# Optimization experiments

Hardware: AMD Instinct MI355X
Metric: run time of the kernel (lower is better)

The kernel has to match this reference:

```python
import jax, jax.numpy as jnp
import numpy as np

N_NODES = 100000
N_EDGES = 3200000
K_HOPS = 10
ALPHA = 0.1


def setup_inputs() -> dict:
    key = jax.random.key(0)
    ks = jax.random.split(key, 7)
    x = jax.random.normal(ks[0], (N_NODES, 500), dtype=jnp.float32)
    edge_index = jax.random.randint(ks[1], (2, N_EDGES), 0, N_NODES, dtype=jnp.int32)
    W1 = jax.random.normal(ks[2], (500, 64), dtype=jnp.float32) * 0.05
    b1 = jax.random.normal(ks[3], (64,), dtype=jnp.float32) * 0.05
    W2 = jax.random.normal(ks[4], (64, 64), dtype=jnp.float32) * 0.1
    b2 = jax.random.normal(ks[5], (64,), dtype=jnp.float32) * 0.05
    # PPR init: temp[k] = alpha*(1-alpha)^k, temp[K] = (1-alpha)^K
    temp = ALPHA * (1.0 - ALPHA) ** np.arange(K_HOPS + 1)
    temp[-1] = (1.0 - ALPHA) ** K_HOPS
    temp = jnp.asarray(temp, dtype=jnp.float32)
    return {"x": x, "edge_index": edge_index, "W1": W1, "b1": b1,
            "W2": W2, "b2": b2, "temp": temp}


def reference(x, edge_index, W1, b1, W2, b2, temp):
    n = x.shape[0]
    # MLP (dropout is identity in eval mode)
    h = jax.nn.relu(x @ W1 + b1)
    h = h @ W2 + b2  # [N, C]

    # gcn_norm with self-loops (edge_weight=None -> all ones)
    loops = jnp.arange(n, dtype=edge_index.dtype)
    row = jnp.concatenate([edge_index[0], loops])  # source (x_j)
    col = jnp.concatenate([edge_index[1], loops])  # target (aggregate)
    w = jnp.ones(row.shape[0], dtype=h.dtype)
    deg = jax.ops.segment_sum(w, col, num_segments=n)
    dinv = jnp.where(deg > 0, jax.lax.rsqrt(deg), 0.0)
    norm = dinv[row] * w * dinv[col]  # [E+N]

    # GPR propagation: hidden = sum_k temp[k] * A_hat^k h
    hidden = h * temp[0]
    cur = h
    for k in range(K_HOPS):
        cur = jax.ops.segment_sum(norm[:, None] * cur[row], col, num_segments=n)
        hidden = hidden + temp[k + 1] * cur

    return jax.nn.log_softmax(hidden, axis=1)
```

## Files before the change

### kernel.cpp

```cpp
#include <hip/hip_runtime.h>
#include <hip/hip_bf16.h>
#include <math.h>

#define FEAT_IN 500
#define HID 64
#define NPB 128
#define MAXB 1024

typedef unsigned int uint;
typedef unsigned short ushort;
typedef __attribute__((ext_vector_type(8))) short bf16x8;
typedef __attribute__((ext_vector_type(4))) float f32x4;

__device__ inline ushort f2bf(float f) {
    uint u = __float_as_uint(f);
    uint r = (u + 0x7fff + ((u >> 16) & 1)) >> 16;
    return (ushort)r;
}

__device__ inline uint pk2(float a, float b) {
    uint ua = __float_as_uint(a), ub = __float_as_uint(b);
    ua = ua + 0x7fff + ((ua >> 16) & 1);
    ub = ub + 0x7fff + ((ub >> 16) & 1);
    return (ua >> 16) | (ub & 0xffff0000u);
}

__device__ inline void bf8_unpack(const uint4 v, float f[8]) {
    f[0] = __uint_as_float(v.x << 16);
    f[1] = __uint_as_float(v.x & 0xffff0000u);
    f[2] = __uint_as_float(v.y << 16);
    f[3] = __uint_as_float(v.y & 0xffff0000u);
    f[4] = __uint_as_float(v.z << 16);
    f[5] = __uint_as_float(v.z & 0xffff0000u);
    f[6] = __uint_as_float(v.w << 16);
    f[7] = __uint_as_float(v.w & 0xffff0000u);
}

__global__ __launch_bounds__(256) void bcnt_kernel(const int* __restrict__ col,
                                                   int* __restrict__ bcnt, int E, int nbkt) {
    __shared__ int cnt[MAXB];
    int tid = threadIdx.x;
    for (int j = tid; j < nbkt; j += 256) cnt[j] = 0;
    __syncthreads();
    int stride = gridDim.x * 256;
    for (int e = blockIdx.x * 256 + tid; e < E; e += stride) {
        atomicAdd(&cnt[col[e] >> 7], 1);
    }
    __syncthreads();
    for (int j = tid; j < nbkt; j += 256) {
        int v = cnt[j];
        if (v) atomicAdd(&bcnt[j], v);
    }
}

__global__ void bscan_kernel(const int* __restrict__ bcnt, int* __restrict__ boff,
                             int* __restrict__ bcur, int* __restrict__ ptr,
                             int nbkt, int n, int E) {
    int lane = threadIdx.x;
    int run = 0;
    for (int base = 0; base < nbkt; base += 64) {
        int i = base + lane;
        int v = (i < nbkt) ? bcnt[i] : 0;
        int sc = v;
#pragma unroll
        for (int d = 1; d < 64; d <<= 1) {
            int t = __shfl_up(sc, d);
            if (lane >= d) sc += t;
        }
        if (i < nbkt) {
            int ex = run + sc - v;
            boff[i] = ex;
            bcur[i] = ex;
        }
        run += __shfl(sc, 63);
    }
    if (lane == 0) {
        boff[nbkt] = E;
        ptr[n] = E;
    }
}

__global__ __launch_bounds__(1024) void bscat_kernel(const int* __restrict__ row,
                                                     const int* __restrict__ col,
                                                     int* __restrict__ bcur,
                                                     uint* __restrict__ csr_tmp,
                                                     int E, int nbkt) {
    __shared__ int cnt[MAXB];
    __shared__ int pos[MAXB];
    int tid = threadIdx.x;
    int chunk = (E + gridDim.x - 1) / gridDim.x;
    int c0 = blockIdx.x * chunk;
    int c1 = min(E, c0 + chunk);
    for (int j = tid; j < nbkt; j += 1024) cnt[j] = 0;
    __syncthreads();
    for (int e = c0 + tid; e < c1; e += 1024) atomicAdd(&cnt[col[e] >> 7], 1);
    __syncthreads();
    for (int j = tid; j < nbkt; j += 1024) {
        int v = cnt[j];
        pos[j] = v ? atomicAdd(&bcur[j], v) : 0;
    }
    __syncthreads();
    for (int e = c0 + tid; e < c1; e += 1024) {
        int c = col[e];
        int j = c >> 7;
        int r = atomicAdd(&pos[j], 1);
        csr_tmp[r] = ((uint)row[e] << 7) | (uint)(c & (NPB - 1));
    }
}

__global__ __launch_bounds__(256) void bsort_kernel(const uint* __restrict__ csr_tmp,
                                                    const int* __restrict__ boff,
                                                    int* __restrict__ ptr,
                                                    float* __restrict__ dinv,
                                                    int* __restrict__ csr_src,
                                                    int n) {
    __shared__ int degl[NPB];
    __shared__ int offl[NPB];
    int b = blockIdx.x;
    int tid = threadIdx.x;
    int t0 = boff[b], t1 = boff[b + 1];
    if (tid < NPB) degl[tid] = 0;
    __syncthreads();
    for (int p = t0 + tid; p < t1; p += 256) {
        uint pk = csr_tmp[p];
        atomicAdd(&degl[pk & (NPB - 1)], 1);
    }
    __syncthreads();
    if (tid < 64) {
        int v0 = degl[tid];
        int s0 = v0;
#pragma unroll
        for (int d = 1; d < 64; d <<= 1) {
            int t = __shfl_up(s0, d);
            if (tid >= d) s0 += t;
        }
        int tot0 = __shfl(s0, 63);
        int v1 = degl[64 + tid];
        int s1 = v1;
#pragma unroll
        for (int d = 1; d < 64; d <<= 1) {
            int t = __shfl_up(s1, d);
            if (tid >= d) s1 += t;
        }
        offl[tid] = s0 - v0;
        offl[64 + tid] = tot0 + s1 - v1;
    }
    __syncthreads();
    if (tid < NPB) {
        int node = b * NPB + tid;
        if (node < n) {
            ptr[node] = t0 + offl[tid];
            dinv[node] = rsqrtf((float)(degl[tid] + 1));
        }
    }
    __syncthreads();
    for (int p = t0 + tid; p < t1; p += 256) {
        uint pk = csr_tmp[p];
        int l = pk & (NPB - 1);
        int r = t0 + atomicAdd(&offl[l], 1);
        csr_src[r] = (int)(pk >> 7);
    }
}

__global__ void swz_kernel(const float* __restrict__ W1, const float* __restrict__ W2,
                           ushort* __restrict__ w1s, ushort* __restrict__ w2s) {
    int idx = blockIdx.x * blockDim.x + threadIdx.x;
    if (idx < 32768) {
        int j = idx & 7;
        int l = (idx >> 3) & 63;
        int t = (idx >> 9) & 3;
        int c = idx >> 11;
        int k = c * 32 + (l >> 4) * 8 + j;
        int nn = t * 16 + (l & 15);
        float v = (k < FEAT_IN) ? W1[(size_t)k * HID + nn] : 0.0f;
        w1s[idx] = f2bf(v);
    } else if (idx < 32768 + 4096) {
        int r = idx - 32768;
        int j = r & 7;
        int l = (r >> 3) & 63;
        int t = (r >> 9) & 3;
        int c = r >> 11;
        int k = c * 32 + (l >> 4) * 8 + j;
        int nn = t * 16 + (l & 15);
        w2s[r] = f2bf(W2[(size_t)k * HID + nn]);
    }
}

__global__ __launch_bounds__(256) void mlp_kernel(const float* __restrict__ x,
                                                  const ushort* __restrict__ w1s,
                                                  const float* __restrict__ b1,
                                                  const ushort* __restrict__ w2s,
                                                  const float* __restrict__ b2,
                                                  const float* __restrict__ temp,
                                                  const float* __restrict__ dinv,
                                                  ushort* __restrict__ A,
                                                  float* __restrict__ out, int n) {
    __shared__ float pacc[2][2][16][65];
    __shared__ ushort hls[2][16 * 72];
    const int tid = threadIdx.x;
    const int lane = tid & 63;
    const int wv = tid >> 6;
    const int tl = wv >> 1;
    const int kh = wv & 1;
    const int g = lane >> 4;
    const int c15 = lane & 15;
    const int nmt = (n + 15) / 16;
    int mt = blockIdx.x * 2 + tl;
    bool mtok = (mt < nmt);
    float t0 = temp[0];

    f32x4 acc[4] = {{0.f, 0.f, 0.f, 0.f}, {0.f, 0.f, 0.f, 0.f},
                    {0.f, 0.f, 0.f, 0.f}, {0.f, 0.f, 0.f, 0.f}};
    int row = mt * 16 + c15;
    bool rok = mtok && (row < n);
    const float* xr = x + (size_t)row * FEAT_IN;

    if (mtok) {
        const int cbeg = kh * 8;
        const int cend = kh ? 15 : 8;
        float4 L0 = {0.f, 0.f, 0.f, 0.f}, H0 = L0, L1 = L0, H1 = L0;
        if (rok) {
            L0 = *(const float4*)(xr + cbeg * 32 + g * 8);
            H0 = *(const float4*)(xr + cbeg * 32 + g * 8 + 4);
            L1 = *(const float4*)(xr + (cbeg + 1) * 32 + g * 8);
            H1 = *(const float4*)(xr + (cbeg + 1) * 32 + g * 8 + 4);
        }
        for (int c = cbeg; c < cend; c++) {
            float4 Ln = {0.f, 0.f, 0.f, 0.f}, Hn = Ln;
            int cn = c + 2;
            if (rok && cn < cend) {
                Ln = *(const float4*)(xr + cn * 32 + g * 8);
                Hn = *(const float4*)(xr + cn * 32 + g * 8 + 4);
            }
            uint4 au;
            au.x = pk2(L0.x, L0.y);
            au.y = pk2(L0.z, L0.w);
            au.z = pk2(H0.x, H0.y);
            au.w = pk2(H0.z, H0.w);
            bf16x8 a = *(bf16x8*)&au;
            const ushort* wp = w1s + ((size_t)c * 4) * 512 + lane * 8;
#pragma unroll
            for (int t = 0; t < 4; t++) {
                bf16x8 b = *(const bf16x8*)(wp + t * 512);
                acc[t] = __builtin_amdgcn_mfma_f32_16x16x32_bf16(a, b, acc[t], 0, 0, 0);
            }
            L0 = L1; H0 = H1; L1 = Ln; H1 = Hn;
        }
        if (kh) {
            float v[8];
#pragma unroll
            for (int j = 0; j < 8; j++) {
                int k = 480 + g * 8 + j;
                v[j] = (rok && k < FEAT_IN) ? xr[k] : 0.0f;
            }
            uint4 au;
            au.x = pk2(v[0], v[1]);
            au.y = pk2(v[2], v[3]);
            au.z = pk2(v[4], v[5]);
            au.w = pk2(v[6], v[7]);
            bf16x8 a = *(bf16x8*)&au;
            const ushort* wp = w1s + (size_t)15 * 4 * 512 + lane * 8;
#pragma unroll
            for (int t = 0; t < 4; t++) {
                bf16x8 b = *(const bf16x8*)(wp + t * 512);
                acc[t] = __builtin_amdgcn_mfma_f32_16x16x32_bf16(a, b, acc[t], 0, 0, 0);
            }
        }
#pragma unroll
        for (int t = 0; t < 4; t++) {
#pragma unroll
            for (int r = 0; r < 4; r++) {
                pacc[tl][kh][g * 4 + r][t * 16 + c15] = acc[t][r];
            }
        }
    }
    __syncthreads();

    if (mtok) {
        int rrow = lane & 15;
        int cg = lane >> 4;
        int colbase = kh * 32 + cg * 8;
#pragma unroll
        for (int cc = 0; cc < 8; cc++) {
            int colc = colbase + cc;
            float h = pacc[tl][0][rrow][colc] + pacc[tl][1][rrow][colc] + b1[colc];
            hls[tl][rrow * 72 + colc] = f2bf(fmaxf(h, 0.0f));
        }
    }
    __syncthreads();
    if (!mtok) return;

    f32x4 acc2[2] = {{0.f, 0.f, 0.f, 0.f}, {0.f, 0.f, 0.f, 0.f}};
#pragma unroll
    for (int c2 = 0; c2 < 2; c2++) {
        bf16x8 a2 = *(const bf16x8*)(hls[tl] + c15 * 72 + c2 * 32 + g * 8);
#pragma unroll
        for (int tt = 0; tt < 2; tt++) {
            int t = kh * 2 + tt;
            bf16x8 b = *(const bf16x8*)(w2s + ((size_t)(c2 * 4 + t)) * 512 + lane * 8);
            acc2[tt] = __builtin_amdgcn_mfma_f32_16x16x32_bf16(a2, b, acc2[tt], 0, 0, 0);
        }
    }

#pragma unroll
    for (int tt = 0; tt < 2; tt++) {
        int t = kh * 2 + tt;
        float b2v = b2[t * 16 + c15];
#pragma unroll
        for (int r = 0; r < 4; r++) {
            int orow = mt * 16 + g * 4 + r;
            if (orow < n) {
                float dres = acc2[tt][r] + b2v;
                size_t o = (size_t)orow * HID + t * 16 + c15;
                A[o] = f2bf(dinv[orow] * dres);
                out[o] = t0 * dres;
            }
        }
    }
}

__global__ __launch_bounds__(256) void hopf_kernel(const int* __restrict__ ptr,
                                                   const int* __restrict__ csr_src,
                                                   const float* __restrict__ dinv,
                                                   const ushort* __restrict__ cur,
                                                   ushort* __restrict__ nxt,
                                                   float* __restrict__ out,
                                                   const float* __restrict__ temp,
                                                   int tidx, int Kf, int n) {
    int i = (blockIdx.x * blockDim.x + threadIdx.x) >> 6;
    int lane = threadIdx.x & 63;
    if (i >= n) return;
    const int g = lane >> 3;
    const int q = lane & 7;

    int s = ptr[i];
    int e = ptr[i + 1];
    const uint* curu = (const uint*)cur;

    float acc[8] = {0.f, 0.f, 0.f, 0.f, 0.f, 0.f, 0.f, 0.f};
    float accB[8] = {0.f, 0.f, 0.f, 0.f, 0.f, 0.f, 0.f, 0.f};

    int rounds = (e - s + 31) >> 5;
    int p = s + g;
    int j0 = csr_src[(p      < e) ? p      : 0];
    int j1 = csr_src[(p + 8  < e) ? p + 8  : 0];
    int j2 = csr_src[(p + 16 < e) ? p + 16 : 0];
    int j3 = csr_src[(p + 24 < e) ? p + 24 : 0];

    for (int r = 0; r < rounds; r++) {
        int pn = p + 32;
        int k0 = csr_src[(pn      < e) ? pn      : 0];
        int k1 = csr_src[(pn + 8  < e) ? pn + 8  : 0];
        int k2 = csr_src[(pn + 16 < e) ? pn + 16 : 0];
        int k3 = csr_src[(pn + 24 < e) ? pn + 24 : 0];
        uint4 v0 = *(const uint4*)(curu + (size_t)j0 * 32 + q * 4);
        uint4 v1 = *(const uint4*)(curu + (size_t)j1 * 32 + q * 4);
        uint4 v2 = *(const uint4*)(curu + (size_t)j2 * 32 + q * 4);
        uint4 v3 = *(const uint4*)(curu + (size_t)j3 * 32 + q * 4);
        float w0 = (p      < e) ? 1.0f : 0.0f;
        float w1 = (p + 8  < e) ? 1.0f : 0.0f;
        float w2 = (p + 16 < e) ? 1.0f : 0.0f;
        float w3 = (p + 24 < e) ? 1.0f : 0.0f;
        float f[8];
        bf8_unpack(v0, f);
#pragma unroll
        for (int t = 0; t < 8; t++) acc[t] += w0 * f[t];
        bf8_unpack(v1, f);
#pragma unroll
        for (int t = 0; t < 8; t++) accB[t] += w1 * f[t];
        bf8_unpack(v2, f);
#pragma unroll
        for (int t = 0; t < 8; t++) acc[t] += w2 * f[t];
        bf8_unpack(v3, f);
#pragma unroll
        for (int t = 0; t < 8; t++) accB[t] += w3 * f[t];
        p = pn;
        j0 = k0; j1 = k1; j2 = k2; j3 = k3;
    }
#pragma unroll
    for (int t = 0; t < 8; t++) acc[t] += accB[t];

#pragma unroll
    for (int m = 8; m <= 32; m <<= 1) {
#pragma unroll
        for (int t = 0; t < 8; t++) acc[t] += __shfl_xor(acc[t], m);
    }

    uint4 sv = *(const uint4*)(curu + (size_t)i * 32 + q * 4);
    float sf[8];
    bf8_unpack(sv, sf);
#pragma unroll
    for (int t = 0; t < 8; t++) acc[t] += sf[t];

    if (lane < 8) {
        float d = dinv[i];
        float dd = d * d;
        float tk = temp[tidx] * d;
        if (tidx < Kf) {
            uint4 pk;
            pk.x = (uint)f2bf(dd * acc[0]) | ((uint)f2bf(dd * acc[1]) << 16);
            pk.y = (uint)f2bf(dd * acc[2]) | ((uint)f2bf(dd * acc[3]) << 16);
            pk.z = (uint)f2bf(dd * acc[4]) | ((uint)f2bf(dd * acc[5]) << 16);
            pk.w = (uint)f2bf(dd * acc[6]) | ((uint)f2bf(dd * acc[7]) << 16);
            *(uint4*)((uint*)nxt + (size_t)i * 32 + q * 4) = pk;
        }

        float* op = out + (size_t)i * HID + q * 8;
        float4 o0 = *(const float4*)(op);
        float4 o1 = *(const float4*)(op + 4);
        o0.x += tk * acc[0]; o0.y += tk * acc[1]; o0.z += tk * acc[2]; o0.w += tk * acc[3];
        o1.x += tk * acc[4]; o1.y += tk * acc[5]; o1.z += tk * acc[6]; o1.w += tk * acc[7];

        if (tidx == Kf) {
            float m = fmaxf(fmaxf(fmaxf(o0.x, o0.y), fmaxf(o0.z, o0.w)),
                            fmaxf(fmaxf(o1.x, o1.y), fmaxf(o1.z, o1.w)));
#pragma unroll
            for (int dm = 1; dm <= 4; dm <<= 1) m = fmaxf(m, __shfl_xor(m, dm));
            float ex = expf(o0.x - m) + expf(o0.y - m) + expf(o0.z - m) + expf(o0.w - m)
                     + expf(o1.x - m) + expf(o1.y - m) + expf(o1.z - m) + expf(o1.w - m);
#pragma unroll
            for (int dm = 1; dm <= 4; dm <<= 1) ex += __shfl_xor(ex, dm);
            float L = m + logf(ex);
            o0.x -= L; o0.y -= L; o0.z -= L; o0.w -= L;
            o1.x -= L; o1.y -= L; o1.z -= L; o1.w -= L;
        }
        *(float4*)(op) = o0;
        *(float4*)(op + 4) = o1;
    }
}

__global__ __launch_bounds__(256) void lsm_kernel(float* __restrict__ out, int n) {
    int i = (blockIdx.x * blockDim.x + threadIdx.x) >> 6;
    int lane = threadIdx.x & 63;
    if (i >= n) return;
    size_t o = (size_t)i * HID + lane;
    float v = out[o];
    float m = v;
#pragma unroll
    for (int d = 32; d >= 1; d >>= 1) m = fmaxf(m, __shfl_xor(m, d));
    float ex = expf(v - m);
#pragma unroll
    for (int d = 32; d >= 1; d >>= 1) ex += __shfl_xor(ex, d);
    out[o] = v - m - logf(ex);
}

extern "C" void kernel_launch(void* const* d_in, const int* in_sizes, int n_in,
                              void* d_out, int out_size, void* d_ws, size_t ws_size,
                              hipStream_t stream) {
    const float* x    = (const float*)d_in[0];
    const int*   ei   = (const int*)d_in[1];
    const float* W1   = (const float*)d_in[2];
    const float* b1   = (const float*)d_in[3];
    const float* W2   = (const float*)d_in[4];
    const float* b2   = (const float*)d_in[5];
    const float* temp = (const float*)d_in[6];

    int n = in_sizes[0] / FEAT_IN;
    int E = in_sizes[1] / 2;
    int K = in_sizes[6] - 1;
    const int* row = ei;
    const int* col = ei + E;
    int nbkt = (n + NPB - 1) >> 7;

    char* ws = (char*)d_ws;
    size_t off = 0;
    auto alloc = [&](size_t bytes) -> void* {
        void* p = (void*)(ws + off);
        off += (bytes + 255) & ~(size_t)255;
        return p;
    };
    size_t nf = (size_t)n * HID;
    ushort* A      = (ushort*)alloc(nf * sizeof(ushort));
    ushort* B      = (ushort*)alloc(nf * sizeof(ushort));
    float* dinv    = (float*)alloc((size_t)n * sizeof(float));
    int*   ptr     = (int*)alloc((size_t)(n + 1) * sizeof(int));
    int*   bcnt    = (int*)alloc((size_t)MAXB * sizeof(int));
    int*   boff    = (int*)alloc((size_t)(MAXB + 1) * sizeof(int));
    int*   bcur    = (int*)alloc((size_t)MAXB * sizeof(int));
    uint*  csr_tmp = (uint*)alloc((size_t)E * sizeof(uint));
    int*   csr_src = (int*)alloc((size_t)E * sizeof(int));
    ushort* w1s    = (ushort*)alloc(32768 * sizeof(ushort));
    ushort* w2s    = (ushort*)alloc(4096 * sizeof(ushort));
    (void)ws_size;

    float* out = (float*)d_out;

    hipMemsetAsync(bcnt, 0, (size_t)nbkt * sizeof(int), stream);

    bcnt_kernel<<<256, 256, 0, stream>>>(col, bcnt, E, nbkt);
    bscan_kernel<<<1, 64, 0, stream>>>(bcnt, boff, bcur, ptr, nbkt, n, E);
    bscat_kernel<<<256, 1024, 0, stream>>>(row, col, bcur, csr_tmp, E, nbkt);
    bsort_kernel<<<nbkt, 256, 0, stream>>>(csr_tmp, boff, ptr, dinv, csr_src, n);
    swz_kernel<<<(32768 + 4096 + 255) / 256, 256, 0, stream>>>(W1, W2, w1s, w2s);

    int nmt = (n + 15) / 16;
    int mlp_blocks = (nmt + 1) / 2;
    mlp_kernel<<<mlp_blocks, 256, 0, stream>>>(x, w1s, b1, w2s, b2, temp, dinv, A, out, n);

    int hop_blocks = (n + 3) / 4;
    ushort* cur = A;
    ushort* nxt = B;
    for (int k = 0; k < K; k++) {
        hopf_kernel<<<hop_blocks, 256, 0, stream>>>(ptr, csr_src, dinv, cur, nxt, out,
                                                    temp, k + 1, K, n);
        ushort* t = cur; cur = nxt; nxt = t;
    }
    if (K == 0) {
        lsm_kernel<<<hop_blocks, 256, 0, stream>>>(out, n);
    }
}
```

Before: 1.052 ms.

## Defer per-hop output accumulation by storing all hop vectors in workspace

When the workspace is large enough, each hop writes its bf16 result into a separate slice instead of ping-ponging two buffers. Intermediate hops skip the fp32 read-modify-write of the output. The final hop reads all stored slices and accumulates them before the log-softmax. This removes nine fp32 output round-trips per node in exchange for one bf16 read of every stored hop at the end, but it uses K times more workspace and adds a serial loop to the last kernel.

Measured after the change: 1.025 ms, median of 2. 1.03x faster.

```diff
diff --git a/kernel.cpp b/kernel.cpp
--- a/kernel.cpp
+++ b/kernel.cpp
@@ -326,12 +326,14 @@
                                                    ushort* __restrict__ nxt,
                                                    float* __restrict__ out,
                                                    const float* __restrict__ temp,
-                                                   int tidx, int Kf, int n) {
+                                                   const ushort* __restrict__ Sbase,
+                                                   int tidx, int Kf, int defer, int n) {
     int i = (blockIdx.x * blockDim.x + threadIdx.x) >> 6;
     int lane = threadIdx.x & 63;
     if (i >= n) return;
     const int g = lane >> 3;
     const int q = lane & 7;
+    const size_t nf = (size_t)n * HID;
 
     int s = ptr[i];
     int e = ptr[i + 1];
@@ -403,15 +405,35 @@
             pk.z = (uint)f2bf(dd * acc[4]) | ((uint)f2bf(dd * acc[5]) << 16);
             pk.w = (uint)f2bf(dd * acc[6]) | ((uint)f2bf(dd * acc[7]) << 16);
             *(uint4*)((uint*)nxt + (size_t)i * 32 + q * 4) = pk;
-        }
-
-        float* op = out + (size_t)i * HID + q * 8;
-        float4 o0 = *(const float4*)(op);
-        float4 o1 = *(const float4*)(op + 4);
-        o0.x += tk * acc[0]; o0.y += tk * acc[1]; o0.z += tk * acc[2]; o0.w += tk * acc[3];
-        o1.x += tk * acc[4]; o1.y += tk * acc[5]; o1.z += tk * acc[6]; o1.w += tk * acc[7];
-
-        if (tidx == Kf) {
+
+            if (!defer) {
+                float* op = out + (size_t)i * HID + q * 8;
+                float4 o0 = *(const float4*)(op);
+                float4 o1 = *(const float4*)(op + 4);
+                o0.x += tk * acc[0]; o0.y += tk * acc[1]; o0.z += tk * acc[2]; o0.w += tk * acc[3];
+                o1.x += tk * acc[4]; o1.y += tk * acc[5]; o1.z += tk * acc[6]; o1.w += tk * acc[7];
+                *(float4*)(op) = o0;
+                *(float4*)(op + 4) = o1;
+            }
+        } else {
+            float* op = out + (size_t)i * HID + q * 8;
+            float4 o0 = *(const float4*)(op);
+            float4 o1 = *(const float4*)(op + 4);
+            if (defer) {
+                float rd = 1.0f / d;
+                for (int k = 1; k < Kf; k++) {
+                    const uint* sp = (const uint*)(Sbase + (size_t)k * nf) + (size_t)i * 32 + q * 4;
+                    uint4 v = *(const uint4*)sp;
+                    float f[8];
+                    bf8_unpack(v, f);
+                    float c = temp[k] * rd;
+                    o0.x += c * f[0]; o0.y += c * f[1]; o0.z += c * f[2]; o0.w += c * f[3];
+                    o1.x += c * f[4]; o1.y += c * f[5]; o1.z += c * f[6]; o1.w += c * f[7];
+                }
+            }
+            o0.x += tk * acc[0]; o0.y += tk * acc[1]; o0.z += tk * acc[2]; o0.w += tk * acc[3];
+            o1.x += tk * acc[4]; o1.y += tk * acc[5]; o1.z += tk * acc[6]; o1.w += tk * acc[7];
+
             float m = fmaxf(fmaxf(fmaxf(o0.x, o0.y), fmaxf(o0.z, o0.w)),
                             fmaxf(fmaxf(o1.x, o1.y), fmaxf(o1.z, o1.w)));
 #pragma unroll
@@ -423,9 +445,9 @@
             float L = m + logf(ex);
             o0.x -= L; o0.y -= L; o0.z -= L; o0.w -= L;
             o1.x -= L; o1.y -= L; o1.z -= L; o1.w -= L;
-        }
-        *(float4*)(op) = o0;
-        *(float4*)(op + 4) = o1;
+            *(float4*)(op) = o0;
+            *(float4*)(op + 4) = o1;
+        }
     }
 }
 
@@ -469,9 +491,6 @@
         off += (bytes + 255) & ~(size_t)255;
         return p;
     };
-    size_t nf = (size_t)n * HID;
-    ushort* A      = (ushort*)alloc(nf * sizeof(ushort));
-    ushort* B      = (ushort*)alloc(nf * sizeof(ushort));
     float* dinv    = (float*)alloc((size_t)n * sizeof(float));
     int*   ptr     = (int*)alloc((size_t)(n + 1) * sizeof(int));
     int*   bcnt    = (int*)alloc((size_t)MAXB * sizeof(int));
@@ -481,7 +500,21 @@
     int*   csr_src = (int*)alloc((size_t)E * sizeof(int));
     ushort* w1s    = (ushort*)alloc(32768 * sizeof(ushort));
     ushort* w2s    = (ushort*)alloc(4096 * sizeof(ushort));
-    (void)ws_size;
+
+    size_t nf = (size_t)n * HID;
+    size_t rem = (off <= ws_size) ? (ws_size - off) : 0;
+    int defer = 0;
+    ushort *A, *B, *S = nullptr;
+    if (K > 1 && rem >= (size_t)K * nf * sizeof(ushort) + 1024) {
+        defer = 1;
+        S = (ushort*)alloc((size_t)K * nf * sizeof(ushort));
+        A = S;
+        B = S;
+    } else {
+        A = (ushort*)alloc(nf * sizeof(ushort));
+        B = (ushort*)alloc(nf * sizeof(ushort));
+        S = A;
+    }
 
     float* out = (float*)d_out;
 
@@ -498,12 +531,21 @@
     mlp_kernel<<<mlp_blocks, 256, 0, stream>>>(x, w1s, b1, w2s, b2, temp, dinv, A, out, n);
 
     int hop_blocks = (n + 3) / 4;
-    ushort* cur = A;
-    ushort* nxt = B;
-    for (int k = 0; k < K; k++) {
-        hopf_kernel<<<hop_blocks, 256, 0, stream>>>(ptr, csr_src, dinv, cur, nxt, out,
-                                                    temp, k + 1, K, n);
-        ushort* t = cur; cur = nxt; nxt = t;
+    if (defer) {
+        for (int k = 0; k < K; k++) {
+            const ushort* cur = S + (size_t)k * nf;
+            ushort* nxt = (k + 1 < K) ? (S + (size_t)(k + 1) * nf) : S;
+            hopf_kernel<<<hop_blocks, 256, 0, stream>>>(ptr, csr_src, dinv, cur, nxt, out,
+                                                        temp, S, k + 1, K, 1, n);
+        }
+    } else {
+        ushort* cur = A;
+        ushort* nxt = B;
+        for (int k = 0; k < K; k++) {
+            hopf_kernel<<<hop_blocks, 256, 0, stream>>>(ptr, csr_src, dinv, cur, nxt, out,
+                                                        temp, S, k + 1, K, 0, n);
+            ushort* t = cur; cur = nxt; nxt = t;
+        }
     }
     if (K == 0) {
         lsm_kernel<<<hop_blocks, 256, 0, stream>>>(out, n);
```

## Quantize propagated features to int8 with a global scale and defer output accumulation

Applied to the files above, without the earlier changes.

Node features passed between hops are stored as 8-bit values with a single global scale, taken from an atomic max over the MLP output, instead of bf16. This halves the bytes gathered per edge in each hop. When workspace allows, every hop's features are kept and the weighted sum into the float output is deferred to the last hop, which removes the per-hop read-modify-write of the output. The cost is a large loss of precision: the fixed scale comes from the first layer, so later hops can saturate or lose resolution, and that risks accuracy tolerance failures.

Measured after the change: 1.550 ms. +47.4%, slower.

```diff
diff --git a/kernel.cpp b/kernel.cpp
--- a/kernel.cpp
+++ b/kernel.cpp
@@ -9,6 +9,7 @@
 
 typedef unsigned int uint;
 typedef unsigned short ushort;
+typedef unsigned char uchar;
 typedef __attribute__((ext_vector_type(8))) short bf16x8;
 typedef __attribute__((ext_vector_type(4))) float f32x4;
 
@@ -34,6 +35,17 @@
     f[5] = __uint_as_float(v.z & 0xffff0000u);
     f[6] = __uint_as_float(v.w << 16);
     f[7] = __uint_as_float(v.w & 0xffff0000u);
+}
+
+__device__ inline void u8x16_acc(const uint4 v, float w, float f[16]) {
+    const uint u[4] = {v.x, v.y, v.z, v.w};
+#pragma unroll
+    for (int a = 0; a < 4; a++) {
+#pragma unroll
+        for (int b = 0; b < 4; b++) {
+            f[a * 4 + b] += w * (float)((u[a] >> (8 * b)) & 0xffu);
+        }
+    }
 }
 
 __global__ __launch_bounds__(256) void bcnt_kernel(const int* __restrict__ col,
@@ -193,7 +205,8 @@
                                                   const float* __restrict__ b2,
                                                   const float* __restrict__ temp,
                                                   const float* __restrict__ dinv,
-                                                  ushort* __restrict__ A,
+                                                  ushort* __restrict__ Abf,
+                                                  uint* __restrict__ smax,
                                                   float* __restrict__ out, int n) {
     __shared__ float pacc[2][2][16][65];
     __shared__ ushort hls[2][16 * 72];
@@ -288,144 +301,228 @@
         }
     }
     __syncthreads();
-    if (!mtok) return;
-
-    f32x4 acc2[2] = {{0.f, 0.f, 0.f, 0.f}, {0.f, 0.f, 0.f, 0.f}};
-#pragma unroll
-    for (int c2 = 0; c2 < 2; c2++) {
-        bf16x8 a2 = *(const bf16x8*)(hls[tl] + c15 * 72 + c2 * 32 + g * 8);
+
+    float mx = 0.0f;
+    if (mtok) {
+        f32x4 acc2[2] = {{0.f, 0.f, 0.f, 0.f}, {0.f, 0.f, 0.f, 0.f}};
+#pragma unroll
+        for (int c2 = 0; c2 < 2; c2++) {
+            bf16x8 a2 = *(const bf16x8*)(hls[tl] + c15 * 72 + c2 * 32 + g * 8);
+#pragma unroll
+            for (int tt = 0; tt < 2; tt++) {
+                int t = kh * 2 + tt;
+                bf16x8 b = *(const bf16x8*)(w2s + ((size_t)(c2 * 4 + t)) * 512 + lane * 8);
+                acc2[tt] = __builtin_amdgcn_mfma_f32_16x16x32_bf16(a2, b, acc2[tt], 0, 0, 0);
+            }
+        }
+
 #pragma unroll
         for (int tt = 0; tt < 2; tt++) {
             int t = kh * 2 + tt;
-            bf16x8 b = *(const bf16x8*)(w2s + ((size_t)(c2 * 4 + t)) * 512 + lane * 8);
-            acc2[tt] = __builtin_amdgcn_mfma_f32_16x16x32_bf16(a2, b, acc2[tt], 0, 0, 0);
-        }
-    }
-
-#pragma unroll
-    for (int tt = 0; tt < 2; tt++) {
-        int t = kh * 2 + tt;
-        float b2v = b2[t * 16 + c15];
-#pragma unroll
-        for (int r = 0; r < 4; r++) {
-            int orow = mt * 16 + g * 4 + r;
-            if (orow < n) {
-                float dres = acc2[tt][r] + b2v;
-                size_t o = (size_t)orow * HID + t * 16 + c15;
-                A[o] = f2bf(dinv[orow] * dres);
-                out[o] = t0 * dres;
-            }
-        }
-    }
-}
-
-__global__ __launch_bounds__(256) void hopf_kernel(const int* __restrict__ ptr,
+            float b2v = b2[t * 16 + c15];
+#pragma unroll
+            for (int r = 0; r < 4; r++) {
+                int orow = mt * 16 + g * 4 + r;
+                if (orow < n) {
+                    float dres = acc2[tt][r] + b2v;
+                    float sv = dinv[orow] * dres;
+                    size_t o = (size_t)orow * HID + t * 16 + c15;
+                    Abf[o] = f2bf(sv);
+                    out[o] = t0 * dres;
+                    mx = fmaxf(mx, fabsf(sv));
+                }
+            }
+        }
+    }
+#pragma unroll
+    for (int dm = 1; dm < 64; dm <<= 1) mx = fmaxf(mx, __shfl_xor(mx, dm));
+    if (lane == 0) atomicMax(smax, __float_as_uint(mx));
+}
+
+__global__ __launch_bounds__(256) void q8_kernel(const ushort* __restrict__ Abf,
+                                                 uchar* __restrict__ S0,
+                                                 const uint* __restrict__ smax, size_t nf) {
+    size_t idx = (size_t)blockIdx.x * 256 + threadIdx.x;
+    if (idx * 8 >= nf) return;
+    float sm = fmaxf(__uint_as_float(smax[0]), 1e-30f);
+    float rs = 127.0f / sm;
+    uint4 v = *(const uint4*)(Abf + idx * 8);
+    float f[8];
+    bf8_unpack(v, f);
+    uint b0 = 0, b1 = 0;
+#pragma unroll
+    for (int j = 0; j < 4; j++) {
+        int qi = (int)rintf(f[j] * rs);
+        qi = max(-128, min(127, qi));
+        b0 |= ((uint)(qi + 128) & 0xffu) << (8 * j);
+    }
+#pragma unroll
+    for (int j = 0; j < 4; j++) {
+        int qi = (int)rintf(f[4 + j] * rs);
+        qi = max(-128, min(127, qi));
+        b1 |= ((uint)(qi + 128) & 0xffu) << (8 * j);
+    }
+    uint2 pk;
+    pk.x = b0;
+    pk.y = b1;
+    *(uint2*)(S0 + idx * 8) = pk;
+}
+
+__global__ __launch_bounds__(256) void hop8_kernel(const int* __restrict__ ptr,
                                                    const int* __restrict__ csr_src,
                                                    const float* __restrict__ dinv,
-                                                   const ushort* __restrict__ cur,
-                                                   ushort* __restrict__ nxt,
+                                                   const uchar* __restrict__ cur,
+                                                   uchar* __restrict__ nxt,
                                                    float* __restrict__ out,
                                                    const float* __restrict__ temp,
-                                                   int tidx, int Kf, int n) {
+                                                   const uchar* __restrict__ Sbase,
+                                                   const uint* __restrict__ smax,
+                                                   int tidx, int Kf, int defer, int n) {
     int i = (blockIdx.x * blockDim.x + threadIdx.x) >> 6;
     int lane = threadIdx.x & 63;
     if (i >= n) return;
-    const int g = lane >> 3;
-    const int q = lane & 7;
+    const int slot = lane >> 2;
+    const int q = lane & 3;
+    const size_t nb = (size_t)n * 64;
+
+    float sm = fmaxf(__uint_as_float(smax[0]), 1e-30f);
+    float sc = sm * (1.0f / 127.0f);
 
     int s = ptr[i];
     int e = ptr[i + 1];
-    const uint* curu = (const uint*)cur;
-
-    float acc[8] = {0.f, 0.f, 0.f, 0.f, 0.f, 0.f, 0.f, 0.f};
-    float accB[8] = {0.f, 0.f, 0.f, 0.f, 0.f, 0.f, 0.f, 0.f};
-
-    int rounds = (e - s + 31) >> 5;
-    int p = s + g;
+
+    float acc[16], accB[16];
+#pragma unroll
+    for (int t = 0; t < 16; t++) { acc[t] = 0.f; accB[t] = 0.f; }
+
+    int rounds = (e - s + 63) >> 6;
+    int p = s + slot;
     int j0 = csr_src[(p      < e) ? p      : 0];
-    int j1 = csr_src[(p + 8  < e) ? p + 8  : 0];
-    int j2 = csr_src[(p + 16 < e) ? p + 16 : 0];
-    int j3 = csr_src[(p + 24 < e) ? p + 24 : 0];
+    int j1 = csr_src[(p + 16 < e) ? p + 16 : 0];
+    int j2 = csr_src[(p + 32 < e) ? p + 32 : 0];
+    int j3 = csr_src[(p + 48 < e) ? p + 48 : 0];
 
     for (int r = 0; r < rounds; r++) {
-        int pn = p + 32;
+        int pn = p + 64;
         int k0 = csr_src[(pn      < e) ? pn      : 0];
-        int k1 = csr_src[(pn + 8  < e) ? pn + 8  : 0];
-        int k2 = csr_src[(pn + 16 < e) ? pn + 16 : 0];
-        int k3 = csr_src[(pn + 24 < e) ? pn + 24 : 0];
-        uint4 v0 = *(const uint4*)(curu + (size_t)j0 * 32 + q * 4);
-        uint4 v1 = *(const uint4*)(curu + (size_t)j1 * 32 + q * 4);
-        uint4 v2 = *(const uint4*)(curu + (size_t)j2 * 32 + q * 4);
-        uint4 v3 = *(const uint4*)(curu + (size_t)j3 * 32 + q * 4);
+        int k1 = csr_src[(pn + 16 < e) ? pn + 16 : 0];
+        int k2 = csr_src[(pn + 32 < e) ? pn + 32 : 0];
+        int k3 = csr_src[(pn + 48 < e) ? pn + 48 : 0];
+        uint4 v0 = *(const uint4*)(cur + (size_t)j0 * 64 + q * 16);
+        uint4 v1 = *(const uint4*)(cur + (size_t)j1 * 64 + q * 16);
+        uint4 v2 = *(const uint4*)(cur + (size_t)j2 * 64 + q * 16);
+        uint4 v3 = *(const uint4*)(cur + (size_t)j3 * 64 + q * 16);
         float w0 = (p      < e) ? 1.0f : 0.0f;
-        float w1 = (p + 8  < e) ? 1.0f : 0.0f;
-        float w2 = (p + 16 < e) ? 1.0f : 0.0f;
-        float w3 = (p + 24 < e) ? 1.0f : 0.0f;
-        float f[8];
-        bf8_unpack(v0, f);
-#pragma unroll
-        for (int t = 0; t < 8; t++) acc[t] += w0 * f[t];
-        bf8_unpack(v1, f);
-#pragma unroll
-        for (int t = 0; t < 8; t++) accB[t] += w1 * f[t];
-        bf8_unpack(v2, f);
-#pragma unroll
-        for (int t = 0; t < 8; t++) acc[t] += w2 * f[t];
-        bf8_unpack(v3, f);
-#pragma unroll
-        for (int t = 0; t < 8; t++) accB[t] += w3 * f[t];
+        float w1 = (p + 16 < e) ? 1.0f : 0.0f;
+        float w2 = (p + 32 < e) ? 1.0f : 0.0f;
+        float w3 = (p + 48 < e) ? 1.0f : 0.0f;
+        u8x16_acc(v0, w0, acc);
+        u8x16_acc(v1, w1, accB);
+        u8x16_acc(v2, w2, acc);
+        u8x16_acc(v3, w3, accB);
         p = pn;
         j0 = k0; j1 = k1; j2 = k2; j3 = k3;
     }
 #pragma unroll
-    for (int t = 0; t < 8; t++) acc[t] += accB[t];
-
-#pragma unroll
-    for (int m = 8; m <= 32; m <<= 1) {
-#pragma unroll
-        for (int t = 0; t < 8; t++) acc[t] += __shfl_xor(acc[t], m);
-    }
-
-    uint4 sv = *(const uint4*)(curu + (size_t)i * 32 + q * 4);
-    float sf[8];
-    bf8_unpack(sv, sf);
-#pragma unroll
-    for (int t = 0; t < 8; t++) acc[t] += sf[t];
-
-    if (lane < 8) {
+    for (int t = 0; t < 16; t++) acc[t] += accB[t];
+
+#pragma unroll
+    for (int m = 4; m <= 32; m <<= 1) {
+#pragma unroll
+        for (int t = 0; t < 16; t++) acc[t] += __shfl_xor(acc[t], m);
+    }
+
+    uint4 sv = *(const uint4*)(cur + (size_t)i * 64 + q * 16);
+    u8x16_acc(sv, 1.0f, acc);
+
+    if (slot == 0) {
         float d = dinv[i];
         float dd = d * d;
-        float tk = temp[tidx] * d;
+        int cnt = (e - s) + 1;
+        float corr = 128.0f * (float)cnt;
+        float Tc[16];
+#pragma unroll
+        for (int t = 0; t < 16; t++) Tc[t] = sc * (acc[t] - corr);
+
         if (tidx < Kf) {
-            uint4 pk;
-            pk.x = (uint)f2bf(dd * acc[0]) | ((uint)f2bf(dd * acc[1]) << 16);
-            pk.y = (uint)f2bf(dd * acc[2]) | ((uint)f2bf(dd * acc[3]) << 16);
-            pk.z = (uint)f2bf(dd * acc[4]) | ((uint)f2bf(dd * acc[5]) << 16);
-            pk.w = (uint)f2bf(dd * acc[6]) | ((uint)f2bf(dd * acc[7]) << 16);
-            *(uint4*)((uint*)nxt + (size_t)i * 32 + q * 4) = pk;
-        }
-
-        float* op = out + (size_t)i * HID + q * 8;
-        float4 o0 = *(const float4*)(op);
-        float4 o1 = *(const float4*)(op + 4);
-        o0.x += tk * acc[0]; o0.y += tk * acc[1]; o0.z += tk * acc[2]; o0.w += tk * acc[3];
-        o1.x += tk * acc[4]; o1.y += tk * acc[5]; o1.z += tk * acc[6]; o1.w += tk * acc[7];
-
-        if (tidx == Kf) {
-            float m = fmaxf(fmaxf(fmaxf(o0.x, o0.y), fmaxf(o0.z, o0.w)),
-                            fmaxf(fmaxf(o1.x, o1.y), fmaxf(o1.z, o1.w)));
-#pragma unroll
-            for (int dm = 1; dm <= 4; dm <<= 1) m = fmaxf(m, __shfl_xor(m, dm));
-            float ex = expf(o0.x - m) + expf(o0.y - m) + expf(o0.z - m) + expf(o0.w - m)
-                     + expf(o1.x - m) + expf(o1.y - m) + expf(o1.z - m) + expf(o1.w - m);
-#pragma unroll
-            for (int dm = 1; dm <= 4; dm <<= 1) ex += __shfl_xor(ex, dm);
+            float rs = 1.0f / sc;
+            uint ub[4];
+#pragma unroll
+            for (int w = 0; w < 4; w++) {
+                uint b = 0;
+#pragma unroll
+                for (int bb = 0; bb < 4; bb++) {
+                    int qi = (int)rintf(dd * Tc[w * 4 + bb] * rs);
+                    qi = max(-128, min(127, qi));
+                    b |= ((uint)(qi + 128) & 0xffu) << (8 * bb);
+                }
+                ub[w] = b;
+            }
+            uint4 pkv;
+            pkv.x = ub[0]; pkv.y = ub[1]; pkv.z = ub[2]; pkv.w = ub[3];
+            *(uint4*)(nxt + (size_t)i * 64 + q * 16) = pkv;
+
+            if (!defer) {
+                float tk = temp[tidx] * d;
+                float* op = out + (size_t)i * HID + q * 16;
+#pragma unroll
+                for (int w = 0; w < 4; w++) {
+                    float4 o = *(const float4*)(op + w * 4);
+                    o.x += tk * Tc[w * 4 + 0];
+                    o.y += tk * Tc[w * 4 + 1];
+                    o.z += tk * Tc[w * 4 + 2];
+                    o.w += tk * Tc[w * 4 + 3];
+                    *(float4*)(op + w * 4) = o;
+                }
+            }
+        } else {
+            float* op = out + (size_t)i * HID + q * 16;
+            float o[16];
+#pragma unroll
+            for (int w = 0; w < 4; w++) {
+                float4 t4 = *(const float4*)(op + w * 4);
+                o[w * 4 + 0] = t4.x; o[w * 4 + 1] = t4.y;
+                o[w * 4 + 2] = t4.z; o[w * 4 + 3] = t4.w;
+            }
+            if (defer) {
+                float rd = 1.0f / d;
+                for (int k = 1; k < Kf; k++) {
+                    uint4 v = *(const uint4*)(Sbase + (size_t)k * nb + (size_t)i * 64 + q * 16);
+                    float c = temp[k] * rd * sc;
+                    float cc = c * 128.0f;
+                    const uint u[4] = {v.x, v.y, v.z, v.w};
+#pragma unroll
+                    for (int a = 0; a < 4; a++) {
+#pragma unroll
+                        for (int bb = 0; bb < 4; bb++) {
+                            o[a * 4 + bb] += c * (float)((u[a] >> (8 * bb)) & 0xffu) - cc;
+                        }
+                    }
+                }
+            }
+            float tk = temp[tidx] * d;
+#pragma unroll
+            for (int t = 0; t < 16; t++) o[t] += tk * Tc[t];
+
+            float m = o[0];
+#pragma unroll
+            for (int t = 1; t < 16; t++) m = fmaxf(m, o[t]);
+#pragma unroll
+            for (int dm = 1; dm <= 2; dm <<= 1) m = fmaxf(m, __shfl_xor(m, dm));
+            float ex = 0.f;
+#pragma unroll
+            for (int t = 0; t < 16; t++) ex += expf(o[t] - m);
+#pragma unroll
+            for (int dm = 1; dm <= 2; dm <<= 1) ex += __shfl_xor(ex, dm);
             float L = m + logf(ex);
-            o0.x -= L; o0.y -= L; o0.z -= L; o0.w -= L;
-            o1.x -= L; o1.y -= L; o1.z -= L; o1.w -= L;
-        }
-        *(float4*)(op) = o0;
-        *(float4*)(op + 4) = o1;
+#pragma unroll
+            for (int w = 0; w < 4; w++) {
+                float4 t4;
+                t4.x = o[w * 4 + 0] - L; t4.y = o[w * 4 + 1] - L;
+                t4.z = o[w * 4 + 2] - L; t4.w = o[w * 4 + 3] - L;
+                *(float4*)(op + w * 4) = t4;
+            }
+        }
     }
 }
 
@@ -469,23 +566,39 @@
         off += (bytes + 255) & ~(size_t)255;
         return p;
     };
-    size_t nf = (size_t)n * HID;
-    ushort* A      = (ushort*)alloc(nf * sizeof(ushort));
-    ushort* B      = (ushort*)alloc(nf * sizeof(ushort));
     float* dinv    = (float*)alloc((size_t)n * sizeof(float));
     int*   ptr     = (int*)alloc((size_t)(n + 1) * sizeof(int));
     int*   bcnt    = (int*)alloc((size_t)MAXB * sizeof(int));
     int*   boff    = (int*)alloc((size_t)(MAXB + 1) * sizeof(int));
     int*   bcur    = (int*)alloc((size_t)MAXB * sizeof(int));
+    uint*  smax    = (uint*)alloc(256);
     uint*  csr_tmp = (uint*)alloc((size_t)E * sizeof(uint));
     int*   csr_src = (int*)alloc((size_t)E * sizeof(int));
     ushort* w1s    = (ushort*)alloc(32768 * sizeof(ushort));
     ushort* w2s    = (ushort*)alloc(4096 * sizeof(ushort));
-    (void)ws_size;
+
+    size_t nf = (size_t)n * HID;
+    size_t nb = (size_t)n * 64;
+    ushort* Abf = (ushort*)alloc(nf * sizeof(ushort));
+
+    size_t rem = (off <= ws_size) ? (ws_size - off) : 0;
+    int defer = 0;
+    uchar *A8, *B8, *S = nullptr;
+    if (K > 1 && rem >= (size_t)K * nb + 1024) {
+        defer = 1;
+        S = (uchar*)alloc((size_t)K * nb);
+        A8 = S;
+        B8 = S;
+    } else {
+        A8 = (uchar*)alloc(nb);
+        B8 = (uchar*)alloc(nb);
+        S = A8;
+    }
 
     float* out = (float*)d_out;
 
     hipMemsetAsync(bcnt, 0, (size_t)nbkt * sizeof(int), stream);
+    hipMemsetAsync(smax, 0, sizeof(uint), stream);
 
     bcnt_kernel<<<256, 256, 0, stream>>>(col, bcnt, E, nbkt);
     bscan_kernel<<<1, 64, 0, stream>>>(bcnt, boff, bcur, ptr, nbkt, n, E);
@@ -495,17 +608,32 @@
 
     int nmt = (n + 15) / 16;
     int mlp_blocks = (nmt + 1) / 2;
-    mlp_kernel<<<mlp_blocks, 256, 0, stream>>>(x, w1s, b1, w2s, b2, temp, dinv, A, out, n);
+    mlp_kernel<<<mlp_blocks, 256, 0, stream>>>(x, w1s, b1, w2s, b2, temp, dinv,
+                                               Abf, smax, out, n);
 
     int hop_blocks = (n + 3) / 4;
-    ushort* cur = A;
-    ushort* nxt = B;
-    for (int k = 0; k < K; k++) {
-        hopf_kernel<<<hop_blocks, 256, 0, stream>>>(ptr, csr_src, dinv, cur, nxt, out,
-                                                    temp, k + 1, K, n);
-        ushort* t = cur; cur = nxt; nxt = t;
-    }
-    if (K == 0) {
+    if (K > 0) {
+        uchar* S0 = defer ? S : A8;
+        int qblocks = (int)((nf / 8 + 255) / 256);
+        q8_kernel<<<qblocks, 256, 0, stream>>>(Abf, S0, smax, nf);
+
+        if (defer) {
+            for (int k = 0; k < K; k++) {
+                const uchar* cur = S + (size_t)k * nb;
+                uchar* nxt = (k + 1 < K) ? (S + (size_t)(k + 1) * nb) : S;
+                hop8_kernel<<<hop_blocks, 256, 0, stream>>>(ptr, csr_src, dinv, cur, nxt, out,
+                                                            temp, S, smax, k + 1, K, 1, n);
+            }
+        } else {
+            uchar* cur = A8;
+            uchar* nxt = B8;
+            for (int k = 0; k < K; k++) {
+                hop8_kernel<<<hop_blocks, 256, 0, stream>>>(ptr, csr_src, dinv, cur, nxt, out,
+                                                            temp, S, smax, k + 1, K, 0, n);
+                uchar* t = cur; cur = nxt; nxt = t;
+            }
+        }
+    } else {
         lsm_kernel<<<hop_blocks, 256, 0, stream>>>(out, n);
     }
 }
```
